# Kernel optimization log

Hardware: AMD Instinct MI355X
Metric: run time of the kernel (lower is better)

## Reference

```python
import jax, jax.numpy as jnp
import numpy as np

H = 16  # num_heads

def setup_inputs() -> dict:
    key = jax.random.key(0)
    ks = jax.random.split(key, 5)
    B, T, C = 2, 2048, 1024
    x = jax.random.normal(ks[0], (B, T, C), dtype=jnp.float32)
    # causal mask: 1 = keep, 0 = mask (masked_fill(mask == 0, -inf))
    mask = jnp.tril(jnp.ones((T, T), dtype=jnp.int32))[None, None]
    s = 1.0 / np.sqrt(C)
    Wqkv = jax.random.normal(ks[1], (C, 3 * C), dtype=jnp.float32) * s
    bqkv = jnp.zeros((3 * C,), dtype=jnp.float32)
    Wo = jax.random.normal(ks[2], (C, C), dtype=jnp.float32) * s
    bo = jnp.zeros((C,), dtype=jnp.float32)
    return {"x": x, "mask": mask, "Wqkv": Wqkv, "bqkv": bqkv, "Wo": Wo, "bo": bo}

def reference(x, mask, Wqkv, bqkv, Wo, bo):
    B, T, C = x.shape
    D = C // H  # head_dim
    qkv = (x @ Wqkv + bqkv).reshape(B, T, 3, H, D)
    q, k, v = qkv[:, :, 0], qkv[:, :, 1], qkv[:, :, 2]  # [B, T, H, D]
    scores = jnp.einsum('bqhd,bkhd->bhqk', q, k) / jnp.sqrt(jnp.asarray(D, x.dtype))
    scores = jnp.where(mask == 0, -jnp.inf, scores)
    attn = jax.nn.softmax(scores, axis=-1)  # dropout p=0.0 -> identity
    ctx = jnp.einsum('bhqk,bkhd->bqhd', attn, v).reshape(B, T, C)
    return ctx @ Wo + bo
```

## Files before the change

kernel.cpp:

```cpp
#include <hip/hip_runtime.h>

typedef unsigned short u16;
typedef unsigned int u32;

using bf16x8 = __attribute__((ext_vector_type(8))) __bf16;
using f32x4  = __attribute__((ext_vector_type(4))) float;

__device__ __forceinline__ u16 f2bf(float f){
  u32 u = __builtin_bit_cast(u32, f);
  return (u16)((u + 0x7FFFu + ((u >> 16) & 1u)) >> 16);
}
__device__ __forceinline__ float bf2f(u16 v){
  u32 u = ((u32)v) << 16; return __builtin_bit_cast(float, u);
}

__device__ __forceinline__ bf16x8 as_bf16x8(uint4 u){
  union { uint4 u; bf16x8 b; } x; x.u = u; return x.b;
}

__device__ __forceinline__ f32x4 mfma16(bf16x8 a, bf16x8 b, f32x4 c){
  return __builtin_amdgcn_mfma_f32_16x16x32_bf16(a, b, c, 0, 0, 0);
}

__device__ __forceinline__ float fexp2(float x){
  float r; asm("v_exp_f32 %0, %1" : "=v"(r) : "v"(x)); return r;
}

__device__ __forceinline__ u32 cvtpk(float a, float b){
  u32 r; asm("v_cvt_pk_bf16_f32 %0, %1, %2" : "=v"(r) : "v"(a), "v"(b)); return r;
}

__device__ __forceinline__ void gload16(const u16* g, u16* l){
  __builtin_amdgcn_global_load_lds(
      (const __attribute__((address_space(1))) u32*)g,
      (__attribute__((address_space(3))) u32*)l, 16, 0, 0);
}

__global__ void prep_kernel(const float* __restrict__ x, u16* __restrict__ xbf,
                            const float* __restrict__ Wqkv, u16* __restrict__ wqkvT,
                            const float* __restrict__ Wo,   u16* __restrict__ woT)
{
  __shared__ float tile[32][33];
  const int bid = blockIdx.x, tid = threadIdx.x;
  if (bid < 2048){
    int i = bid * 256 + tid;
    const float4* p = (const float4*)x;
    float4 a = p[2*i], b = p[2*i+1];
    uint4 r;
    r.x = (u32)f2bf(a.x) | ((u32)f2bf(a.y) << 16);
    r.y = (u32)f2bf(a.z) | ((u32)f2bf(a.w) << 16);
    r.z = (u32)f2bf(b.x) | ((u32)f2bf(b.y) << 16);
    r.w = (u32)f2bf(b.z) | ((u32)f2bf(b.w) << 16);
    ((uint4*)xbf)[i] = r;
    return;
  }
  const float* in; u16* out; int K, N, tt;
  if (bid < 5120){ in = Wqkv; out = wqkvT; K = 1024; N = 3072; tt = bid - 2048; }
  else           { in = Wo;   out = woT;   K = 1024; N = 1024; tt = bid - 5120; }
  const int nbx = N >> 5;
  const int n0 = (tt % nbx) * 32, k0 = (tt / nbx) * 32;
  const int tx = tid & 31, ty = tid >> 5;
  #pragma unroll
  for (int j = 0; j < 32; j += 8)
    tile[ty + j][tx] = in[(size_t)(k0 + ty + j) * N + n0 + tx];
  __syncthreads();
  #pragma unroll
  for (int j = 0; j < 32; j += 8)
    out[(size_t)(n0 + ty + j) * K + k0 + tx] = f2bf(tile[tx][ty + j]);
}

#define BM 128
#define BK 64

template<int EPI, int NF>
__global__ __launch_bounds__(256, 3) void gemm_bt_kernel(
    const u16* __restrict__ A, const u16* __restrict__ Bt,
    const float* __restrict__ bias,
    u16* __restrict__ Qw, u16* __restrict__ Kw, u16* __restrict__ Vw,
    float* __restrict__ outf, int M, int N, int Kd)
{
  constexpr int BNx = 32 * NF;
  __shared__ __align__(16) u16 As[BM * BK];
  __shared__ __align__(16) u16 Bs[BNx * BK];
  const int tid = threadIdx.x;
  const int w = tid >> 6, lane = tid & 63;
  const int r15 = lane & 15, g = lane >> 4;
  const int bm = blockIdx.y * BM, bn = blockIdx.x * BNx;
  const int wm = (w >> 1) * 64, wn = (w & 1) * (16 * NF);
  const int lr = lane >> 3, lc = lane & 7;
  const int gsw = ((lc ^ lr) * 8);

  const int ntiles = Kd / BK;

  f32x4 acc[4][NF];
  #pragma unroll
  for (int m = 0; m < 4; ++m)
    #pragma unroll
    for (int n = 0; n < NF; ++n)
      acc[m][n] = (f32x4){0.f, 0.f, 0.f, 0.f};

  for (int t = 0; t < ntiles; ++t){
    int k0 = t * BK;
    #pragma unroll
    for (int p = 0; p < 4; ++p){
      int row0 = w * 32 + p * 8;
      gload16(A + (size_t)(bm + row0 + lr) * Kd + k0 + gsw, &As[row0 * BK]);
    }
    #pragma unroll
    for (int p = 0; p < NF; ++p){
      int row0 = w * (8 * NF) + p * 8;
      gload16(Bt + (size_t)(bn + row0 + lr) * Kd + k0 + gsw, &Bs[row0 * BK]);
    }
    __syncthreads();
    #pragma unroll
    for (int kc = 0; kc < 2; ++kc){
      bf16x8 af[4], bfr[NF];
      #pragma unroll
      for (int m = 0; m < 4; ++m){
        int rowa = wm + m * 16 + r15;
        af[m]  = as_bf16x8(*(const uint4*)&As[rowa * BK + (((kc*4 + g) ^ (rowa & 7)) * 8)]);
      }
      #pragma unroll
      for (int n = 0; n < NF; ++n){
        int rowb = wn + n * 16 + r15;
        bfr[n] = as_bf16x8(*(const uint4*)&Bs[rowb * BK + (((kc*4 + g) ^ (rowb & 7)) * 8)]);
      }
      #pragma unroll
      for (int m = 0; m < 4; ++m)
        #pragma unroll
        for (int n = 0; n < NF; ++n)
          acc[m][n] = mfma16(af[m], bfr[n], acc[m][n]);
    }
    __syncthreads();
  }

  if constexpr (EPI == 0){
    const float QSC = 0.18033688011112042f;
    const int sidx_blk = (bn + wn) >> 10;
    if (sidx_blk == 2){
      const int rowbase = bm + wm;
      const int bb = rowbase >> 11;
      const int tb = rowbase & 2047 & ~63;
      #pragma unroll
      for (int ni = 0; ni < NF; ++ni){
        int col = bn + wn + ni * 16 + r15;
        float bv = bias[col];
        int rem = col & 1023, hh = rem >> 6, dd = rem & 63;
        u16* vbase = Vw + (((size_t)(bb * 16 + hh) * 64) + dd) * 2048 + tb + g * 8;
        #pragma unroll
        for (int mh = 0; mh < 2; ++mh){
          uint4 pu;
          pu.x = cvtpk(acc[2*mh  ][ni][0] + bv, acc[2*mh  ][ni][1] + bv);
          pu.y = cvtpk(acc[2*mh  ][ni][2] + bv, acc[2*mh  ][ni][3] + bv);
          pu.z = cvtpk(acc[2*mh+1][ni][0] + bv, acc[2*mh+1][ni][1] + bv);
          pu.w = cvtpk(acc[2*mh+1][ni][2] + bv, acc[2*mh+1][ni][3] + bv);
          *(uint4*)(vbase + mh * 32) = pu;
        }
      }
    } else {
      #pragma unroll
      for (int ni = 0; ni < NF; ++ni){
        int col = bn + wn + ni * 16 + r15;
        float bv = bias[col];
        int rem = col & 1023, hh = rem >> 6, dd = rem & 63;
        #pragma unroll
        for (int mi = 0; mi < 4; ++mi)
          #pragma unroll
          for (int i = 0; i < 4; ++i){
            int row = bm + wm + mi * 16 + 4 * g + i;
            int bb = row >> 11, tt = row & 2047;
            float av = acc[mi][ni][i] + bv;
            if (sidx_blk == 0)
              Qw[(((size_t)(bb * 16 + hh) * 2048) + tt) * 64 + dd] = f2bf(av * QSC);
            else
              Kw[(((size_t)(bb * 16 + hh) * 2048) + tt) * 64 + dd] = f2bf(av);
          }
      }
    }
  } else {
    #pragma unroll
    for (int ni = 0; ni < NF; ++ni){
      int col = bn + wn + ni * 16 + r15;
      float bv = bias[col];
      #pragma unroll
      for (int mi = 0; mi < 4; ++mi)
        #pragma unroll
        for (int i = 0; i < 4; ++i){
          int row = bm + wm + mi * 16 + 4 * g + i;
          outf[(size_t)row * N + col] = acc[mi][ni][i] + bv;
        }
    }
  }
}

#define T_SEQ 2048
#define DH 64

__global__ __launch_bounds__(256, 4) void attn_kernel(
    const u16* __restrict__ Q, const u16* __restrict__ K, const u16* __restrict__ Vt,
    u16* __restrict__ ctx, u16* __restrict__ poB, float* __restrict__ plB)
{
  __shared__ __align__(16) u16 Ks[2][64 * 64];
  __shared__ __align__(16) u16 Vs[2][64 * 64];
  const int tid = threadIdx.x;
  const int w = tid >> 6, lane = tid & 63;
  const int r15 = lane & 15, g = lane >> 4;
  const int lr = lane >> 3, lc = lane & 7;
  const int gsw = ((lc ^ lr) * 8);
  bf16x8 ones;
  { union { uint4 u; bf16x8 b; } x; x.u = make_uint4(0x3F803F80u,0x3F803F80u,0x3F803F80u,0x3F803F80u); ones = x.b; }

  const int id = blockIdx.x;
  const int j = id >> 3;
  const int bh = (id & 7) * 4 + j / 30;
  const int li = j % 30;
  int qt, ci, nc;
  if (li < 6)       { qt = li;                 ci = 0;           nc = 1; }
  else if (li < 18) { qt = 6 + ((li - 6) >> 1); ci = (li - 6) & 1; nc = 2; }
  else              { qt = 12 + (li - 18) / 3;  ci = (li - 18) % 3; nc = 3; }
  const int niter = 2 * qt + 2;
  const int kb = (niter * ci) / nc, ke = (niter * (ci + 1)) / nc;
  const int pidx = bh * 24 + ((qt < 12) ? (qt - 6) * 2 : 12 + (qt - 12) * 3) + ci;

  const int b = bh >> 4, h = bh & 15;
  const u16* Qb = Q  + (size_t)bh * T_SEQ * DH;
  const u16* Kb = K  + (size_t)bh * T_SEQ * DH;
  const u16* Vb = Vt + (size_t)bh * DH * T_SEQ;
  const int q0 = qt * 128, qw = q0 + w * 32;

  bf16x8 qf[2][2];
  #pragma unroll
  for (int rb = 0; rb < 2; ++rb)
    #pragma unroll
    for (int kc = 0; kc < 2; ++kc)
      qf[rb][kc] = as_bf16x8(*(const uint4*)(Qb + (size_t)(qw + rb*16 + r15) * DH + kc*32 + g*8));

  f32x4 o[2][4];
  f32x4 lacc[2];
  #pragma unroll
  for (int rb = 0; rb < 2; ++rb){
    lacc[rb] = (f32x4){0.f,0.f,0.f,0.f};
    #pragma unroll
    for (int dn = 0; dn < 4; ++dn) o[rb][dn] = (f32x4){0.f,0.f,0.f,0.f};
  }

  auto stage = [&](int kt, int buf){
    int k0 = kt * 64;
    #pragma unroll
    for (int p = 0; p < 2; ++p){
      int row0 = w * 16 + p * 8;
      gload16(Kb + (size_t)(k0 + row0 + lr) * DH + gsw,    &Ks[buf][row0 * 64]);
      gload16(Vb + (size_t)(row0 + lr) * T_SEQ + k0 + gsw, &Vs[buf][row0 * 64]);
    }
  };

  stage(kb, 0);
  int cb = 0;
  for (int kt = kb; kt < ke; ++kt){
    asm volatile("s_waitcnt vmcnt(0)" ::: "memory");
    __builtin_amdgcn_sched_barrier(0);
    __builtin_amdgcn_s_barrier();
    __builtin_amdgcn_sched_barrier(0);
    if (kt + 1 < ke) stage(kt + 1, cb ^ 1);
    const int kvb = kt * 64 - q0;
    if (kvb < qw - q0 + 32){
      f32x4 st[2][4];
      #pragma unroll
      for (int rb = 0; rb < 2; ++rb)
        #pragma unroll
        for (int ntv = 0; ntv < 4; ++ntv) st[rb][ntv] = (f32x4){0.f,0.f,0.f,0.f};
      __builtin_amdgcn_s_setprio(1);
      #pragma unroll
      for (int kc = 0; kc < 2; ++kc)
        #pragma unroll
        for (int ntv = 0; ntv < 4; ++ntv){
          int rowk = ntv * 16 + r15;
          bf16x8 kf = as_bf16x8(*(const uint4*)&Ks[cb][rowk * 64 + (((kc*4 + g) ^ (rowk & 7)) * 8)]);
          st[0][ntv] = mfma16(kf, qf[0][kc], st[0][ntv]);
          st[1][ntv] = mfma16(kf, qf[1][kc], st[1][ntv]);
        }
      __builtin_amdgcn_s_setprio(0);
      if (kvb >= 0){
        #pragma unroll
        for (int rb = 0; rb < 2; ++rb)
          #pragma unroll
          for (int ntv = 0; ntv < 4; ++ntv){
            #pragma unroll
            for (int i = 0; i < 4; ++i)
              if (kvb + ntv * 16 + 4 * g + i > (w * 32 + rb * 16 + r15)) st[rb][ntv][i] = -1e30f;
          }
      }
      #pragma unroll
      for (int rb = 0; rb < 2; ++rb)
        #pragma unroll
        for (int ntv = 0; ntv < 4; ++ntv)
          #pragma unroll
          for (int i = 0; i < 4; ++i)
            st[rb][ntv][i] = fexp2(st[rb][ntv][i]);
      __builtin_amdgcn_s_setprio(1);
      #pragma unroll
      for (int kc = 0; kc < 2; ++kc){
        bf16x8 pa[2];
        #pragma unroll
        for (int rb = 0; rb < 2; ++rb){
          uint4 pu;
          pu.x = cvtpk(st[rb][2*kc    ][0], st[rb][2*kc    ][1]);
          pu.y = cvtpk(st[rb][2*kc    ][2], st[rb][2*kc    ][3]);
          pu.z = cvtpk(st[rb][2*kc + 1][0], st[rb][2*kc + 1][1]);
          pu.w = cvtpk(st[rb][2*kc + 1][2], st[rb][2*kc + 1][3]);
          pa[rb] = as_bf16x8(pu);
        }
        lacc[0] = mfma16(pa[0], ones, lacc[0]);
        lacc[1] = mfma16(pa[1], ones, lacc[1]);
        #pragma unroll
        for (int dn = 0; dn < 4; ++dn){
          int rv = dn * 16 + r15;
          bf16x8 vf = as_bf16x8(*(const uint4*)&Vs[cb][rv * 64 + (((kc*4 + g) ^ (rv & 7)) * 8)]);
          o[0][dn] = mfma16(pa[0], vf, o[0][dn]);
          o[1][dn] = mfma16(pa[1], vf, o[1][dn]);
        }
      }
      __builtin_amdgcn_s_setprio(0);
    }
    asm volatile("s_waitcnt lgkmcnt(0)" ::: "memory");
    __builtin_amdgcn_sched_barrier(0);
    cb ^= 1;
  }
  if (nc > 1){
    u16* po = poB + (size_t)pidx * 8192;
    float* pl = plB + (size_t)pidx * 128;
    #pragma unroll
    for (int rb = 0; rb < 2; ++rb){
      #pragma unroll
      for (int dn = 0; dn < 4; ++dn)
        #pragma unroll
        for (int i = 0; i < 4; ++i){
          int row = w * 32 + rb * 16 + 4 * g + i;
          po[row * 64 + dn * 16 + r15] = f2bf(o[rb][dn][i]);
        }
      if (r15 == 0)
        #pragma unroll
        for (int i = 0; i < 4; ++i)
          pl[w * 32 + rb * 16 + 4 * g + i] = lacc[rb][i];
    }
  } else {
    #pragma unroll
    for (int rb = 0; rb < 2; ++rb){
      float rinv[4];
      #pragma unroll
      for (int i = 0; i < 4; ++i) rinv[i] = 1.0f / lacc[rb][i];
      #pragma unroll
      for (int dn = 0; dn < 4; ++dn)
        #pragma unroll
        for (int i = 0; i < 4; ++i){
          int t = qw + rb * 16 + 4 * g + i;
          ctx[((size_t)(b * T_SEQ + t)) * 1024 + h * 64 + dn * 16 + r15] = f2bf(o[rb][dn][i] * rinv[i]);
        }
    }
  }
}

__global__ void combine_kernel(const u16* __restrict__ poB, const float* __restrict__ plB,
                               u16* __restrict__ ctx)
{
  const int cq = blockIdx.x >> 5, bh = blockIdx.x & 31;
  const int qt = 6 + cq;
  const int nc = (qt < 12) ? 2 : 3;
  const int pb = bh * 24 + ((qt < 12) ? (qt - 6) * 2 : 12 + (qt - 12) * 3);
  const int b = bh >> 4, h = bh & 15;
  const int tid = threadIdx.x;
  const int r = tid >> 1, ch = (tid & 1) * 32;
  float lsum = 0.f;
  #pragma unroll 3
  for (int c = 0; c < nc; ++c) lsum += plB[(size_t)(pb + c) * 128 + r];
  const float rinv = 1.0f / lsum;
  float acc[32];
  #pragma unroll
  for (int j = 0; j < 32; ++j) acc[j] = 0.f;
  #pragma unroll 3
  for (int c = 0; c < nc; ++c){
    const u16* p = poB + (size_t)(pb + c) * 8192 + r * 64 + ch;
    #pragma unroll
    for (int q = 0; q < 4; ++q){
      uint4 v0 = *(const uint4*)(p + q * 8);
      u32 vv[4] = {v0.x, v0.y, v0.z, v0.w};
      #pragma unroll
      for (int j = 0; j < 4; ++j){
        acc[q*8 + 2*j    ] += bf2f((u16)(vv[j] & 0xffffu));
        acc[q*8 + 2*j + 1] += bf2f((u16)(vv[j] >> 16));
      }
    }
  }
  u32 ov[16];
  #pragma unroll
  for (int j = 0; j < 16; ++j)
    ov[j] = cvtpk(acc[2*j] * rinv, acc[2*j+1] * rinv);
  u16* dst = ctx + ((size_t)(b * T_SEQ + qt * 128 + r)) * 1024 + h * 64 + ch;
  *(uint4*)(dst     ) = make_uint4(ov[0],  ov[1],  ov[2],  ov[3]);
  *(uint4*)(dst +  8) = make_uint4(ov[4],  ov[5],  ov[6],  ov[7]);
  *(uint4*)(dst + 16) = make_uint4(ov[8],  ov[9],  ov[10], ov[11]);
  *(uint4*)(dst + 24) = make_uint4(ov[12], ov[13], ov[14], ov[15]);
}

extern "C" void kernel_launch(void* const* d_in, const int* in_sizes, int n_in,
                              void* d_out, int out_size, void* d_ws, size_t ws_size,
                              hipStream_t stream) {
  const float* x    = (const float*)d_in[0];
  const float* Wqkv = (const float*)d_in[2];
  const float* bqkv = (const float*)d_in[3];
  const float* Wo   = (const float*)d_in[4];
  const float* bo   = (const float*)d_in[5];
  float* out = (float*)d_out;

  char* ws = (char*)d_ws;
  u16*   xbf   = (u16*)(ws);
  u16*   wqkvT = (u16*)(ws + (size_t)( 8u << 20));
  u16*   woT   = (u16*)(ws + (size_t)(14u << 20));
  u16*   qws   = (u16*)(ws + (size_t)(16u << 20));
  u16*   kws   = (u16*)(ws + (size_t)(24u << 20));
  u16*   vws   = (u16*)(ws + (size_t)(32u << 20));
  u16*   poB   = (u16*)(ws);
  float* plB   = (float*)(ws + (size_t)(13u << 20));
  u16*   ctx   = (u16*)(ws + (size_t)(40u << 20));

  prep_kernel<<<6144, 256, 0, stream>>>(x, xbf, Wqkv, wqkvT, Wo, woT);
  gemm_bt_kernel<0,4><<<dim3(24, 32), 256, 0, stream>>>(xbf, wqkvT, bqkv,
      qws, kws, vws, nullptr, 4096, 3072, 1024);
  attn_kernel<<<960, 256, 0, stream>>>(qws, kws, vws, ctx, poB, plB);
  combine_kernel<<<320, 256, 0, stream>>>(poB, plB, ctx);
  gemm_bt_kernel<1,2><<<dim3(16, 32), 256, 0, stream>>>(ctx, woT, bo,
      nullptr, nullptr, nullptr, out, 4096, 1024, 1024);
  (void)in_sizes; (void)n_in; (void)out_size; (void)ws_size;
}
```

Baseline: 94.80 us.

## Load K/V fragments directly from global into registers, drop LDS staging

Removes the double-buffered LDS staging of K and V tiles, along with the per-iteration barriers and waitcnts. Each wave now loads its own K and V MFMA fragments straight from global memory into registers every iteration, and occupancy launch bounds are lowered from 4 to 2. This avoids LDS traffic and block-wide synchronisation. In exchange, all four waves fetch the same K/V data redundantly from global/L2, the loads are no longer prefetched ahead of use, and register pressure rises.

Result: slower. 145.2 us (+53.1%).

```diff
diff --git a/kernel.cpp b/kernel.cpp
--- a/kernel.cpp
+++ b/kernel.cpp
@@ -196,17 +196,13 @@
 #define T_SEQ 2048
 #define DH 64
 
-__global__ __launch_bounds__(256, 4) void attn_kernel(
+__global__ __launch_bounds__(256, 2) void attn_kernel(
     const u16* __restrict__ Q, const u16* __restrict__ K, const u16* __restrict__ Vt,
     u16* __restrict__ ctx, u16* __restrict__ poB, float* __restrict__ plB)
 {
-  __shared__ __align__(16) u16 Ks[2][64 * 64];
-  __shared__ __align__(16) u16 Vs[2][64 * 64];
   const int tid = threadIdx.x;
   const int w = tid >> 6, lane = tid & 63;
   const int r15 = lane & 15, g = lane >> 4;
-  const int lr = lane >> 3, lc = lane & 7;
-  const int gsw = ((lc ^ lr) * 8);
   bf16x8 ones;
   { union { uint4 u; bf16x8 b; } x; x.u = make_uint4(0x3F803F80u,0x3F803F80u,0x3F803F80u,0x3F803F80u); ones = x.b; }
 
@@ -244,25 +240,20 @@
     for (int dn = 0; dn < 4; ++dn) o[rb][dn] = (f32x4){0.f,0.f,0.f,0.f};
   }
 
-  auto stage = [&](int kt, int buf){
-    int k0 = kt * 64;
-    #pragma unroll
-    for (int p = 0; p < 2; ++p){
-      int row0 = w * 16 + p * 8;
-      gload16(Kb + (size_t)(k0 + row0 + lr) * DH + gsw,    &Ks[buf][row0 * 64]);
-      gload16(Vb + (size_t)(row0 + lr) * T_SEQ + k0 + gsw, &Vs[buf][row0 * 64]);
-    }
-  };
-
-  stage(kb, 0);
-  int cb = 0;
   for (int kt = kb; kt < ke; ++kt){
-    asm volatile("s_waitcnt vmcnt(0)" ::: "memory");
-    __builtin_amdgcn_sched_barrier(0);
-    __builtin_amdgcn_s_barrier();
-    __builtin_amdgcn_sched_barrier(0);
-    if (kt + 1 < ke) stage(kt + 1, cb ^ 1);
-    const int kvb = kt * 64 - q0;
+    const int k0 = kt * 64;
+    const int kvb = k0 - q0;
+    uint4 kfr[8], vfr[8];
+    #pragma unroll
+    for (int c = 0; c < 8; ++c){
+      int kc = c >> 2, ntv = c & 3;
+      kfr[c] = *(const uint4*)(Kb + (size_t)(k0 + ntv*16 + r15) * 64 + kc*32 + g*8);
+    }
+    #pragma unroll
+    for (int c = 0; c < 8; ++c){
+      int kc = c >> 2, dn = c & 3;
+      vfr[c] = *(const uint4*)(Vb + (size_t)(dn*16 + r15) * 2048 + k0 + (kc*4 + g)*8);
+    }
     if (kvb < qw - q0 + 32){
       f32x4 st[2][4];
       #pragma unroll
@@ -274,8 +265,7 @@
       for (int kc = 0; kc < 2; ++kc)
         #pragma unroll
         for (int ntv = 0; ntv < 4; ++ntv){
-          int rowk = ntv * 16 + r15;
-          bf16x8 kf = as_bf16x8(*(const uint4*)&Ks[cb][rowk * 64 + (((kc*4 + g) ^ (rowk & 7)) * 8)]);
+          bf16x8 kf = as_bf16x8(kfr[kc*4 + ntv]);
           st[0][ntv] = mfma16(kf, qf[0][kc], st[0][ntv]);
           st[1][ntv] = mfma16(kf, qf[1][kc], st[1][ntv]);
         }
@@ -314,17 +304,13 @@
         lacc[1] = mfma16(pa[1], ones, lacc[1]);
         #pragma unroll
         for (int dn = 0; dn < 4; ++dn){
-          int rv = dn * 16 + r15;
-          bf16x8 vf = as_bf16x8(*(const uint4*)&Vs[cb][rv * 64 + (((kc*4 + g) ^ (rv & 7)) * 8)]);
+          bf16x8 vf = as_bf16x8(vfr[kc*4 + dn]);
           o[0][dn] = mfma16(pa[0], vf, o[0][dn]);
           o[1][dn] = mfma16(pa[1], vf, o[1][dn]);
         }
       }
       __builtin_amdgcn_s_setprio(0);
     }
-    asm volatile("s_waitcnt lgkmcnt(0)" ::: "memory");
-    __builtin_amdgcn_sched_barrier(0);
-    cb ^= 1;
   }
   if (nc > 1){
     u16* po = poB + (size_t)pidx * 8192;
```
